# Optimization experiments

Measured on AMD Instinct MI355X. Metric: run time of the kernel, lower is better.

## Reference

```python
import jax, jax.numpy as jnp
import numpy as np

EPS = 1e-12  # matches F.normalize eps
K = 256      # prototype_num


def _l2norm(v, axis=-1):
    n = jnp.linalg.norm(v, axis=axis, keepdims=True)
    return v / jnp.maximum(n, EPS)


def setup_inputs() -> dict:
    key = jax.random.key(0)
    k1, k2, k3, k4 = jax.random.split(key, 4)
    B, N, D = 8, 16384, 768
    x = jax.random.normal(k1, (B, N, D), dtype=jnp.float32)
    prototypes = jax.random.normal(k2, (K, D), dtype=jnp.float32)
    W = jax.random.normal(k3, (D, D), dtype=jnp.float32) * (1.0 / np.sqrt(D))
    b = jax.random.normal(k4, (D,), dtype=jnp.float32) * 0.01
    return {"x": x, "prototypes": prototypes, "W": W, "b": b}


def reference(x, prototypes, W, b):
    # cosine similarity: (B,N,D) x (K,D) -> (B,N,K)
    sim = jnp.einsum('bnd,kd->bnk', _l2norm(x), _l2norm(prototypes))
    prob = jax.nn.softmax(sim, axis=-1)
    # weighted prototype mixture, scaled by 1/prototype_num
    x_proto = jnp.einsum('bnk,kd->bnd', prob, prototypes) / K
    # final linear projection (PyTorch Linear: x @ W.T + b)
    return jnp.einsum('bnd,ed->bne', x_proto, W) + b
```

## Files before the change

### kernel.cpp

```cpp
#include <hip/hip_runtime.h>
#include <hip/hip_bf16.h>

typedef unsigned short u16;
typedef __attribute__((ext_vector_type(8))) short bf16x8;
typedef __attribute__((ext_vector_type(4))) float f32x4;

__device__ __forceinline__ u16 f32_to_bf16(float f) {
  unsigned int x = __float_as_uint(f);
  x += 0x7fffu + ((x >> 16) & 1u);
  return (u16)(x >> 16);
}

__global__ __launch_bounds__(256) void prep_pn_kernel(const float* __restrict__ P,
                                                      u16* __restrict__ pn_sw) {
  const int n = blockIdx.x;
  const int t = threadIdx.x;
  float v0 = P[n * 768 + t];
  float v1 = P[n * 768 + t + 256];
  float v2 = P[n * 768 + t + 512];
  float ss = v0 * v0 + v1 * v1 + v2 * v2;
#pragma unroll
  for (int m = 1; m < 64; m <<= 1) ss += __shfl_xor(ss, m, 64);
  __shared__ float wsum[4];
  if ((t & 63) == 0) wsum[t >> 6] = ss;
  __syncthreads();
  const float inv = 1.0f / fmaxf(sqrtf(wsum[0] + wsum[1] + wsum[2] + wsum[3]), 1e-12f);
  float vv[3] = {v0, v1, v2};
#pragma unroll
  for (int i = 0; i < 3; ++i) {
    int d = t + i * 256;
    int c = d >> 5, q = (d >> 3) & 3, j = d & 7;
    pn_sw[c * 8192 + n * 32 + q * 8 + j] = f32_to_bf16(vv[i] * inv);
  }
}

__global__ __launch_bounds__(256) void prep_pw_kernel(const float* __restrict__ P,
                                                      const float* __restrict__ W,
                                                      u16* __restrict__ pw_sw) {
  const int e0 = blockIdx.x * 4;
  const int t = threadIdx.x;
  __shared__ float Wl[4 * 768];
#pragma unroll
  for (int i = 0; i < 12; ++i) Wl[t + i * 256] = W[e0 * 768 + t + i * 256];
  __syncthreads();
  const float* prow = P + t * 768;
  float a0 = 0.f, a1 = 0.f, a2 = 0.f, a3 = 0.f;
  for (int d = 0; d < 768; d += 4) {
    float4 p = *(const float4*)(prow + d);
    a0 += p.x * Wl[d] + p.y * Wl[d + 1] + p.z * Wl[d + 2] + p.w * Wl[d + 3];
    a1 += p.x * Wl[768 + d] + p.y * Wl[768 + d + 1] + p.z * Wl[768 + d + 2] + p.w * Wl[768 + d + 3];
    a2 += p.x * Wl[1536 + d] + p.y * Wl[1536 + d + 1] + p.z * Wl[1536 + d + 2] + p.w * Wl[1536 + d + 3];
    a3 += p.x * Wl[2304 + d] + p.y * Wl[2304 + d + 1] + p.z * Wl[2304 + d + 2] + p.w * Wl[2304 + d + 3];
  }
  const int s = t >> 5, q = (t >> 3) & 3, j8 = t & 7;
  const float sc = 1.0f / 256.0f;
  float av[4] = {a0, a1, a2, a3};
#pragma unroll
  for (int j = 0; j < 4; ++j)
    pw_sw[((s * 768 + e0 + j) * 4 + q) * 8 + j8] = f32_to_bf16(av[j] * sc);
}

__global__ __launch_bounds__(256, 2) void fused_kernel(const float* __restrict__ x,
                                                       const u16* __restrict__ pn_sw,
                                                       const u16* __restrict__ pw_sw,
                                                       const float* __restrict__ bias,
                                                       float* __restrict__ out) {
  __shared__ u16 xn[32 * 776];
  __shared__ u16 probL[32 * 264];
  __shared__ float invn[32];
  __shared__ float rmax[2][32];
  __shared__ float rsum[2][32];

  const int t = threadIdx.x;
  const int w = t >> 6;
  const int lane = t & 63;
  const int r = lane & 15, q = lane >> 4;
  const long row0 = (long)blockIdx.x * 32;

  {
    const int row = t >> 3, s8 = t & 7;
    const float4* xr = (const float4*)(x + (row0 + row) * 768);
    float ss = 0.f;
#pragma unroll
    for (int j = 0; j < 24; ++j) {
      float4 f = xr[s8 + j * 8];
      ss += f.x * f.x + f.y * f.y + f.z * f.z + f.w * f.w;
      ushort4 u;
      u.x = f32_to_bf16(f.x); u.y = f32_to_bf16(f.y);
      u.z = f32_to_bf16(f.z); u.w = f32_to_bf16(f.w);
      *(ushort4*)&xn[row * 776 + (s8 + j * 8) * 4] = u;
    }
    ss += __shfl_xor(ss, 1, 8);
    ss += __shfl_xor(ss, 2, 8);
    ss += __shfl_xor(ss, 4, 8);
    if (s8 == 0) invn[row] = 1.0f / fmaxf(sqrtf(ss), 1e-12f);
  }
  __syncthreads();

  const int rt = w >> 1, ch = w & 1;
  f32x4 acc[8];
#pragma unroll
  for (int ct = 0; ct < 8; ++ct) acc[ct] = f32x4{0.f, 0.f, 0.f, 0.f};
  const u16* aP = &xn[(rt * 16 + r) * 776 + q * 8];
  const u16* bP = pn_sw + (ch * 128 + r) * 32 + q * 8;
#pragma unroll 4
  for (int c = 0; c < 24; ++c) {
    bf16x8 a = *(const bf16x8*)(aP + c * 32);
#pragma unroll
    for (int ct = 0; ct < 8; ++ct) {
      bf16x8 b = *(const bf16x8*)(bP + c * 8192 + ct * 512);
      acc[ct] = __builtin_amdgcn_mfma_f32_16x16x32_bf16(a, b, acc[ct], 0, 0, 0);
    }
  }

  const int rbase = rt * 16 + q * 4;
#pragma unroll
  for (int i = 0; i < 4; ++i) {
    float m = acc[0][i];
#pragma unroll
    for (int ct = 1; ct < 8; ++ct) m = fmaxf(m, acc[ct][i]);
    m = fmaxf(m, __shfl_xor(m, 1, 16));
    m = fmaxf(m, __shfl_xor(m, 2, 16));
    m = fmaxf(m, __shfl_xor(m, 4, 16));
    m = fmaxf(m, __shfl_xor(m, 8, 16));
    if (r == 0) rmax[ch][rbase + i] = m;
  }
  __syncthreads();
#pragma unroll
  for (int i = 0; i < 4; ++i) {
    const float mx = fmaxf(rmax[0][rbase + i], rmax[1][rbase + i]);
    const float inv = invn[rbase + i];
    float s = 0.f;
#pragma unroll
    for (int ct = 0; ct < 8; ++ct) {
      float e = __expf((acc[ct][i] - mx) * inv);
      acc[ct][i] = e;
      s += e;
    }
    s += __shfl_xor(s, 1, 16);
    s += __shfl_xor(s, 2, 16);
    s += __shfl_xor(s, 4, 16);
    s += __shfl_xor(s, 8, 16);
    if (r == 0) rsum[ch][rbase + i] = s;
  }
  __syncthreads();
#pragma unroll
  for (int i = 0; i < 4; ++i) {
    const float isum = 1.0f / (rsum[0][rbase + i] + rsum[1][rbase + i]);
#pragma unroll
    for (int ct = 0; ct < 8; ++ct)
      probL[(rbase + i) * 264 + ch * 128 + ct * 16 + r] = f32_to_bf16(acc[ct][i] * isum);
  }
  __syncthreads();

  const u16* aQ0 = &probL[r * 264 + q * 8];
  const u16* aQ1 = &probL[(16 + r) * 264 + q * 8];
  for (int pass = 0; pass < 3; ++pass) {
    const int e0 = w * 192 + pass * 64;
    f32x4 o0[4], o1[4];
#pragma unroll
    for (int ct = 0; ct < 4; ++ct) {
      o0[ct] = f32x4{0.f, 0.f, 0.f, 0.f};
      o1[ct] = f32x4{0.f, 0.f, 0.f, 0.f};
    }
#pragma unroll
    for (int s = 0; s < 8; ++s) {
      bf16x8 a0 = *(const bf16x8*)(aQ0 + s * 32);
      bf16x8 a1 = *(const bf16x8*)(aQ1 + s * 32);
#pragma unroll
      for (int ct = 0; ct < 4; ++ct) {
        bf16x8 b = *(const bf16x8*)(pw_sw + ((s * 768 + e0 + ct * 16 + r) * 4 + q) * 8);
        o0[ct] = __builtin_amdgcn_mfma_f32_16x16x32_bf16(a0, b, o0[ct], 0, 0, 0);
        o1[ct] = __builtin_amdgcn_mfma_f32_16x16x32_bf16(a1, b, o1[ct], 0, 0, 0);
      }
    }
#pragma unroll
    for (int ct = 0; ct < 4; ++ct) {
      const int e = e0 + ct * 16 + r;
      const float bv = bias[e];
#pragma unroll
      for (int i = 0; i < 4; ++i) {
        out[(row0 + q * 4 + i) * 768 + e] = o0[ct][i] + bv;
        out[(row0 + 16 + q * 4 + i) * 768 + e] = o1[ct][i] + bv;
      }
    }
  }
}

extern "C" void kernel_launch(void* const* d_in, const int* in_sizes, int n_in,
                              void* d_out, int out_size, void* d_ws, size_t ws_size,
                              hipStream_t stream) {
  const float* x = (const float*)d_in[0];
  const float* P = (const float*)d_in[1];
  const float* W = (const float*)d_in[2];
  const float* b = (const float*)d_in[3];
  float* out = (float*)d_out;

  u16* pn_sw = (u16*)d_ws;
  u16* pw_sw = (u16*)d_ws + 256 * 768;

  hipLaunchKernelGGL(prep_pn_kernel, dim3(256), dim3(256), 0, stream, P, pn_sw);
  hipLaunchKernelGGL(prep_pw_kernel, dim3(192), dim3(256), 0, stream, P, W, pw_sw);
  hipLaunchKernelGGL(fused_kernel, dim3(4096), dim3(256), 0, stream, x, pn_sw, pw_sw, b, out);
}
```

Before: 973.4 us.

## Repartition sim GEMM across waves, alias prob buffer, prefetch B operands

The similarity GEMM is re-split so each wave covers all 32 rows and 64 prototypes. Each B fragment loaded from global memory now feeds two MFMAs instead of one, halving per-wave global B traffic, and the softmax reductions widen to four waves. The prob buffer now reuses the xn shared memory, which cuts LDS per block so launch bounds can ask for 3 blocks per CU. B operands for both GEMMs are software-prefetched one k-step ahead in registers, which raises register pressure at the higher occupancy target.

Result: faster. 829.5 us (-14.8%).

```diff
diff --git a/kernel.cpp b/kernel.cpp
--- a/kernel.cpp
+++ b/kernel.cpp
@@ -60,16 +60,16 @@
     pw_sw[((s * 768 + e0 + j) * 4 + q) * 8 + j8] = f32_to_bf16(av[j] * sc);
 }
 
-__global__ __launch_bounds__(256, 2) void fused_kernel(const float* __restrict__ x,
+__global__ __launch_bounds__(256, 3) void fused_kernel(const float* __restrict__ x,
                                                        const u16* __restrict__ pn_sw,
                                                        const u16* __restrict__ pw_sw,
                                                        const float* __restrict__ bias,
                                                        float* __restrict__ out) {
   __shared__ u16 xn[32 * 776];
-  __shared__ u16 probL[32 * 264];
   __shared__ float invn[32];
-  __shared__ float rmax[2][32];
-  __shared__ float rsum[2][32];
+  __shared__ float rmax[4][32];
+  __shared__ float rsum[4][32];
+  u16* probL = xn;
 
   const int t = threadIdx.x;
   const int w = t >> 6;
@@ -95,61 +95,110 @@
     ss += __shfl_xor(ss, 4, 8);
     if (s8 == 0) invn[row] = 1.0f / fmaxf(sqrtf(ss), 1e-12f);
   }
-  __syncthreads();
-
-  const int rt = w >> 1, ch = w & 1;
-  f32x4 acc[8];
-#pragma unroll
-  for (int ct = 0; ct < 8; ++ct) acc[ct] = f32x4{0.f, 0.f, 0.f, 0.f};
-  const u16* aP = &xn[(rt * 16 + r) * 776 + q * 8];
-  const u16* bP = pn_sw + (ch * 128 + r) * 32 + q * 8;
+
+  const u16* bP = pn_sw + (w * 64 + r) * 32 + q * 8;
+  bf16x8 cb0 = *(const bf16x8*)(bP);
+  bf16x8 cb1 = *(const bf16x8*)(bP + 512);
+  bf16x8 cb2 = *(const bf16x8*)(bP + 1024);
+  bf16x8 cb3 = *(const bf16x8*)(bP + 1536);
+  __syncthreads();
+
+  f32x4 accA[4], accB[4];
+#pragma unroll
+  for (int ct = 0; ct < 4; ++ct) {
+    accA[ct] = f32x4{0.f, 0.f, 0.f, 0.f};
+    accB[ct] = f32x4{0.f, 0.f, 0.f, 0.f};
+  }
+  const u16* aP0 = &xn[r * 776 + q * 8];
+  const u16* aP1 = &xn[(16 + r) * 776 + q * 8];
 #pragma unroll 4
-  for (int c = 0; c < 24; ++c) {
-    bf16x8 a = *(const bf16x8*)(aP + c * 32);
-#pragma unroll
-    for (int ct = 0; ct < 8; ++ct) {
-      bf16x8 b = *(const bf16x8*)(bP + c * 8192 + ct * 512);
-      acc[ct] = __builtin_amdgcn_mfma_f32_16x16x32_bf16(a, b, acc[ct], 0, 0, 0);
-    }
-  }
-
-  const int rbase = rt * 16 + q * 4;
+  for (int c = 0; c < 23; ++c) {
+    bf16x8 nb0 = *(const bf16x8*)(bP + (c + 1) * 8192);
+    bf16x8 nb1 = *(const bf16x8*)(bP + (c + 1) * 8192 + 512);
+    bf16x8 nb2 = *(const bf16x8*)(bP + (c + 1) * 8192 + 1024);
+    bf16x8 nb3 = *(const bf16x8*)(bP + (c + 1) * 8192 + 1536);
+    bf16x8 a0 = *(const bf16x8*)(aP0 + c * 32);
+    bf16x8 a1 = *(const bf16x8*)(aP1 + c * 32);
+    accA[0] = __builtin_amdgcn_mfma_f32_16x16x32_bf16(a0, cb0, accA[0], 0, 0, 0);
+    accB[0] = __builtin_amdgcn_mfma_f32_16x16x32_bf16(a1, cb0, accB[0], 0, 0, 0);
+    accA[1] = __builtin_amdgcn_mfma_f32_16x16x32_bf16(a0, cb1, accA[1], 0, 0, 0);
+    accB[1] = __builtin_amdgcn_mfma_f32_16x16x32_bf16(a1, cb1, accB[1], 0, 0, 0);
+    accA[2] = __builtin_amdgcn_mfma_f32_16x16x32_bf16(a0, cb2, accA[2], 0, 0, 0);
+    accB[2] = __builtin_amdgcn_mfma_f32_16x16x32_bf16(a1, cb2, accB[2], 0, 0, 0);
+    accA[3] = __builtin_amdgcn_mfma_f32_16x16x32_bf16(a0, cb3, accA[3], 0, 0, 0);
+    accB[3] = __builtin_amdgcn_mfma_f32_16x16x32_bf16(a1, cb3, accB[3], 0, 0, 0);
+    cb0 = nb0; cb1 = nb1; cb2 = nb2; cb3 = nb3;
+  }
+  {
+    bf16x8 a0 = *(const bf16x8*)(aP0 + 23 * 32);
+    bf16x8 a1 = *(const bf16x8*)(aP1 + 23 * 32);
+    accA[0] = __builtin_amdgcn_mfma_f32_16x16x32_bf16(a0, cb0, accA[0], 0, 0, 0);
+    accB[0] = __builtin_amdgcn_mfma_f32_16x16x32_bf16(a1, cb0, accB[0], 0, 0, 0);
+    accA[1] = __builtin_amdgcn_mfma_f32_16x16x32_bf16(a0, cb1, accA[1], 0, 0, 0);
+    accB[1] = __builtin_amdgcn_mfma_f32_16x16x32_bf16(a1, cb1, accB[1], 0, 0, 0);
+    accA[2] = __builtin_amdgcn_mfma_f32_16x16x32_bf16(a0, cb2, accA[2], 0, 0, 0);
+    accB[2] = __builtin_amdgcn_mfma_f32_16x16x32_bf16(a1, cb2, accB[2], 0, 0, 0);
+    accA[3] = __builtin_amdgcn_mfma_f32_16x16x32_bf16(a0, cb3, accA[3], 0, 0, 0);
+    accB[3] = __builtin_amdgcn_mfma_f32_16x16x32_bf16(a1, cb3, accB[3], 0, 0, 0);
+  }
+
+  const int rbA = q * 4;
 #pragma unroll
   for (int i = 0; i < 4; ++i) {
-    float m = acc[0][i];
-#pragma unroll
-    for (int ct = 1; ct < 8; ++ct) m = fmaxf(m, acc[ct][i]);
-    m = fmaxf(m, __shfl_xor(m, 1, 16));
-    m = fmaxf(m, __shfl_xor(m, 2, 16));
-    m = fmaxf(m, __shfl_xor(m, 4, 16));
-    m = fmaxf(m, __shfl_xor(m, 8, 16));
-    if (r == 0) rmax[ch][rbase + i] = m;
+    float mA = fmaxf(fmaxf(accA[0][i], accA[1][i]), fmaxf(accA[2][i], accA[3][i]));
+    float mB = fmaxf(fmaxf(accB[0][i], accB[1][i]), fmaxf(accB[2][i], accB[3][i]));
+    mA = fmaxf(mA, __shfl_xor(mA, 1, 16));
+    mA = fmaxf(mA, __shfl_xor(mA, 2, 16));
+    mA = fmaxf(mA, __shfl_xor(mA, 4, 16));
+    mA = fmaxf(mA, __shfl_xor(mA, 8, 16));
+    mB = fmaxf(mB, __shfl_xor(mB, 1, 16));
+    mB = fmaxf(mB, __shfl_xor(mB, 2, 16));
+    mB = fmaxf(mB, __shfl_xor(mB, 4, 16));
+    mB = fmaxf(mB, __shfl_xor(mB, 8, 16));
+    if (r == 0) {
+      rmax[w][rbA + i] = mA;
+      rmax[w][16 + rbA + i] = mB;
+    }
   }
   __syncthreads();
 #pragma unroll
   for (int i = 0; i < 4; ++i) {
-    const float mx = fmaxf(rmax[0][rbase + i], rmax[1][rbase + i]);
-    const float inv = invn[rbase + i];
-    float s = 0.f;
-#pragma unroll
-    for (int ct = 0; ct < 8; ++ct) {
-      float e = __expf((acc[ct][i] - mx) * inv);
-      acc[ct][i] = e;
-      s += e;
-    }
-    s += __shfl_xor(s, 1, 16);
-    s += __shfl_xor(s, 2, 16);
-    s += __shfl_xor(s, 4, 16);
-    s += __shfl_xor(s, 8, 16);
-    if (r == 0) rsum[ch][rbase + i] = s;
+    const int rowA = rbA + i, rowB = 16 + rbA + i;
+    const float mxA = fmaxf(fmaxf(rmax[0][rowA], rmax[1][rowA]), fmaxf(rmax[2][rowA], rmax[3][rowA]));
+    const float mxB = fmaxf(fmaxf(rmax[0][rowB], rmax[1][rowB]), fmaxf(rmax[2][rowB], rmax[3][rowB]));
+    const float ivA = invn[rowA], ivB = invn[rowB];
+    float sA = 0.f, sB = 0.f;
+#pragma unroll
+    for (int ct = 0; ct < 4; ++ct) {
+      float eA = __expf((accA[ct][i] - mxA) * ivA);
+      float eB = __expf((accB[ct][i] - mxB) * ivB);
+      accA[ct][i] = eA; accB[ct][i] = eB;
+      sA += eA; sB += eB;
+    }
+    sA += __shfl_xor(sA, 1, 16);
+    sA += __shfl_xor(sA, 2, 16);
+    sA += __shfl_xor(sA, 4, 16);
+    sA += __shfl_xor(sA, 8, 16);
+    sB += __shfl_xor(sB, 1, 16);
+    sB += __shfl_xor(sB, 2, 16);
+    sB += __shfl_xor(sB, 4, 16);
+    sB += __shfl_xor(sB, 8, 16);
+    if (r == 0) {
+      rsum[w][rowA] = sA;
+      rsum[w][rowB] = sB;
+    }
   }
   __syncthreads();
 #pragma unroll
   for (int i = 0; i < 4; ++i) {
-    const float isum = 1.0f / (rsum[0][rbase + i] + rsum[1][rbase + i]);
-#pragma unroll
-    for (int ct = 0; ct < 8; ++ct)
-      probL[(rbase + i) * 264 + ch * 128 + ct * 16 + r] = f32_to_bf16(acc[ct][i] * isum);
+    const int rowA = rbA + i, rowB = 16 + rbA + i;
+    const float isA = 1.0f / (rsum[0][rowA] + rsum[1][rowA] + rsum[2][rowA] + rsum[3][rowA]);
+    const float isB = 1.0f / (rsum[0][rowB] + rsum[1][rowB] + rsum[2][rowB] + rsum[3][rowB]);
+#pragma unroll
+    for (int ct = 0; ct < 4; ++ct) {
+      probL[rowA * 264 + w * 64 + ct * 16 + r] = f32_to_bf16(accA[ct][i] * isA);
+      probL[rowB * 264 + w * 64 + ct * 16 + r] = f32_to_bf16(accB[ct][i] * isB);
+    }
   }
   __syncthreads();
 
@@ -157,6 +206,10 @@
   const u16* aQ1 = &probL[(16 + r) * 264 + q * 8];
   for (int pass = 0; pass < 3; ++pass) {
     const int e0 = w * 192 + pass * 64;
+    bf16x8 bb0 = *(const bf16x8*)(pw_sw + ((e0 + r) * 4 + q) * 8);
+    bf16x8 bb1 = *(const bf16x8*)(pw_sw + ((e0 + 16 + r) * 4 + q) * 8);
+    bf16x8 bb2 = *(const bf16x8*)(pw_sw + ((e0 + 32 + r) * 4 + q) * 8);
+    bf16x8 bb3 = *(const bf16x8*)(pw_sw + ((e0 + 48 + r) * 4 + q) * 8);
     f32x4 o0[4], o1[4];
 #pragma unroll
     for (int ct = 0; ct < 4; ++ct) {
@@ -167,12 +220,22 @@
     for (int s = 0; s < 8; ++s) {
       bf16x8 a0 = *(const bf16x8*)(aQ0 + s * 32);
       bf16x8 a1 = *(const bf16x8*)(aQ1 + s * 32);
-#pragma unroll
-      for (int ct = 0; ct < 4; ++ct) {
-        bf16x8 b = *(const bf16x8*)(pw_sw + ((s * 768 + e0 + ct * 16 + r) * 4 + q) * 8);
-        o0[ct] = __builtin_amdgcn_mfma_f32_16x16x32_bf16(a0, b, o0[ct], 0, 0, 0);
-        o1[ct] = __builtin_amdgcn_mfma_f32_16x16x32_bf16(a1, b, o1[ct], 0, 0, 0);
+      bf16x8 n0, n1, n2, n3;
+      if (s < 7) {
+        n0 = *(const bf16x8*)(pw_sw + (((s + 1) * 768 + e0 + r) * 4 + q) * 8);
+        n1 = *(const bf16x8*)(pw_sw + (((s + 1) * 768 + e0 + 16 + r) * 4 + q) * 8);
+        n2 = *(const bf16x8*)(pw_sw + (((s + 1) * 768 + e0 + 32 + r) * 4 + q) * 8);
+        n3 = *(const bf16x8*)(pw_sw + (((s + 1) * 768 + e0 + 48 + r) * 4 + q) * 8);
       }
+      o0[0] = __builtin_amdgcn_mfma_f32_16x16x32_bf16(a0, bb0, o0[0], 0, 0, 0);
+      o1[0] = __builtin_amdgcn_mfma_f32_16x16x32_bf16(a1, bb0, o1[0], 0, 0, 0);
+      o0[1] = __builtin_amdgcn_mfma_f32_16x16x32_bf16(a0, bb1, o0[1], 0, 0, 0);
+      o1[1] = __builtin_amdgcn_mfma_f32_16x16x32_bf16(a1, bb1, o1[1], 0, 0, 0);
+      o0[2] = __builtin_amdgcn_mfma_f32_16x16x32_bf16(a0, bb2, o0[2], 0, 0, 0);
+      o1[2] = __builtin_amdgcn_mfma_f32_16x16x32_bf16(a1, bb2, o1[2], 0, 0, 0);
+      o0[3] = __builtin_amdgcn_mfma_f32_16x16x32_bf16(a0, bb3, o0[3], 0, 0, 0);
+      o1[3] = __builtin_amdgcn_mfma_f32_16x16x32_bf16(a1, bb3, o1[3], 0, 0, 0);
+      if (s < 7) { bb0 = n0; bb1 = n1; bb2 = n2; bb3 = n3; }
     }
 #pragma unroll
     for (int ct = 0; ct < 4; ++ct) {
```
